# Optimization experiments

Hardware: AMD Instinct MI355X
Metric: run time of the kernel (lower is better)

## Reference

```python
import jax, jax.numpy as jnp
import numpy as np

NUM_GRAPHS = 32   # point clouds per batch
PTS = 1024        # points per cloud (equal-size graphs; batch = node_idx // PTS)
NUM_FEAT = 14
DIM = 64
K = 30            # kNN includes the self-edge (distance 0), as torch_cluster.knn does


def _edge_conv(xb, W1, b1, W2, b2):
    # xb: [B, P, F] node features, per-graph dynamic kNN EdgeConv with max aggregation
    s = jnp.sum(xb * xb, axis=-1)                                   # [B, P]
    d = s[:, :, None] + s[:, None, :] - 2.0 * jnp.einsum('bpf,bqf->bpq', xb, xb)
    idx = jax.lax.top_k(-d, K)[1]                                   # [B, P, K]
    xj = jax.vmap(lambda xg, ig: xg[ig])(xb, idx)                   # [B, P, K, F]
    xi = xb[:, :, None, :]
    e = jnp.concatenate([jnp.broadcast_to(xi, xj.shape), xj - xi], axis=-1)  # [B,P,K,2F]
    h = jax.nn.relu(e @ W1 + b1)
    h = jax.nn.relu(h @ W2 + b2)
    return jnp.max(h, axis=2)                                       # [B, P, DIM]


def setup_inputs() -> dict:
    key = jax.random.key(0)
    ks = jax.random.split(key, 24)
    N = NUM_GRAPHS * PTS

    def w(i, shape):
        scale = shape[0] ** -0.5 if len(shape) > 1 else 0.02
        return jax.random.normal(ks[i], shape, jnp.float32) * scale

    return dict(
        x=jax.random.normal(ks[0], (N, NUM_FEAT), jnp.float32),
        batch=jnp.arange(N, dtype=jnp.int32) // PTS,
        c1w1=w(1, (2 * NUM_FEAT, DIM)), c1b1=w(2, (DIM,)), c1w2=w(3, (DIM, DIM)), c1b2=w(4, (DIM,)),
        c2w1=w(5, (2 * DIM, DIM)), c2b1=w(6, (DIM,)), c2w2=w(7, (DIM, DIM)), c2b2=w(8, (DIM,)),
        c3w1=w(9, (2 * DIM, DIM)), c3b1=w(10, (DIM,)), c3w2=w(11, (DIM, DIM)), c3b2=w(12, (DIM,)),
        lw=w(13, (3 * DIM, 1024)), lb=w(14, (1024,)),
        hw1=w(15, (1024, 256)), hb1=w(16, (256,)),
        hw2=w(17, (256, 128)), hb2=w(18, (128,)),
        hw3=w(19, (128, DIM)), hb3=w(20, (DIM,)),
    )


def reference(x, batch, c1w1, c1b1, c1w2, c1b2, c2w1, c2b1, c2w2, c2b2,
              c3w1, c3b1, c3w2, c3b2, lw, lb, hw1, hb1, hw2, hb2, hw3, hb3):
    # batch encodes equal-size graphs of PTS nodes -> reshape to [B, P, F]
    xb = x.reshape(NUM_GRAPHS, PTS, -1)
    x1 = _edge_conv(xb, c1w1, c1b1, c1w2, c1b2)
    x2 = _edge_conv(x1, c2w1, c2b1, c2w2, c2b2)
    x3 = _edge_conv(x2, c3w1, c3b1, c3w2, c3b2)
    h = jnp.concatenate([x1, x2, x3], axis=-1).reshape(-1, 3 * DIM)  # [N, 192]
    h = jax.nn.relu(h @ lw + lb)      # lin1: MLP([3*dim, 1024])
    h = jax.nn.relu(h @ hw1 + hb1)    # MLP([1024, 256]); dropout = identity at eval
    h = jax.nn.relu(h @ hw2 + hb2)    # MLP([256, 128]); dropout = identity at eval
    return h @ hw3 + hb3              # Lin(128, dim)
```

## Files before the change

### kernel.cpp

```cpp
#include <hip/hip_runtime.h>
#include <hip/hip_bf16.h>
#include <float.h>

#define NG    32
#define PTS   1024
#define NPTS  (NG*PTS)
#define KNN   30
#define DIM   64
#define CHUNK 8192

typedef __attribute__((ext_vector_type(8))) short bf16x8;
typedef __attribute__((ext_vector_type(4))) float f32x4;
typedef unsigned short ushort_t;

__device__ inline void bfsplit(float v, ushort_t& h, ushort_t& l) {
    __hip_bfloat16 bh = __float2bfloat16(v);
    float r = v - __bfloat162float(bh);
    __hip_bfloat16 bl = __float2bfloat16(r);
    h = *reinterpret_cast<ushort_t*>(&bh);
    l = *reinterpret_cast<ushort_t*>(&bl);
}

template<int F>
__global__ __launch_bounds__(256) void prep_k(const float* __restrict__ X, int ldx,
                                              float* __restrict__ S32,
                                              double* __restrict__ S64,
                                              float* __restrict__ XT) {
    int p = blockIdx.x * 256 + threadIdx.x;
    float s32 = 0.f;
    double s64 = 0.0;
    #pragma unroll
    for (int f = 0; f < F; ++f) {
        float v = X[(size_t)p * ldx + f];
        s32 = fmaf(v, v, s32);
        s64 = fma((double)v, (double)v, s64);
        XT[(size_t)f * NPTS + p] = v;
    }
    S32[p] = s32;
    S64[p] = s64;
}

__global__ __launch_bounds__(256) void smax_k(const float* __restrict__ S32,
                                              float* __restrict__ SMAX,
                                              int* __restrict__ ovf_cnt) {
    if (blockIdx.x == 0 && threadIdx.x == 0) *ovf_cnt = 0;
    int g = blockIdx.x;
    int lane = threadIdx.x & 63, wv = threadIdx.x >> 6;
    float m = 0.f;
    for (int t = threadIdx.x; t < PTS; t += 256) m = fmaxf(m, S32[(size_t)g * PTS + t]);
    #pragma unroll
    for (int off = 32; off; off >>= 1) m = fmaxf(m, __shfl_xor(m, off));
    __shared__ float wm[4];
    if (lane == 0) wm[wv] = m;
    __syncthreads();
    if (threadIdx.x == 0)
        SMAX[g] = fmaxf(fmaxf(wm[0], wm[1]), fmaxf(wm[2], wm[3]));
}

template<int F>
__global__ __launch_bounds__(256) void knn_k(const float* __restrict__ X, int ldx,
                                             const float* __restrict__ XT,
                                             const float* __restrict__ S32,
                                             const double* __restrict__ S64,
                                             const float* __restrict__ SMAX,
                                             int* __restrict__ IDX,
                                             int* __restrict__ ovf_cnt,
                                             int* __restrict__ ovf_list) {
    constexpr int FP = (F + 3) & ~3;
    int wv = threadIdx.x >> 6;
    int lane = threadIdx.x & 63;
    int i0 = blockIdx.x * 16;
    int base = i0 & ~(PTS - 1);
    __shared__ __align__(16) float xis[16][FP];
    __shared__ int surv[4][4][64];
    for (int l = threadIdx.x; l < 16 * F; l += 256) {
        int pt = l / F, f = l - pt * F;
        xis[pt][f] = X[(size_t)(i0 + pt) * ldx + f];
    }
    __syncthreads();

    float si[4];
    #pragma unroll
    for (int ii = 0; ii < 4; ++ii) si[ii] = S32[i0 + wv * 4 + ii];
    float smax = SMAX[i0 >> 10];

    float d32[4][16];
    #pragma unroll
    for (int ii = 0; ii < 4; ++ii)
        #pragma unroll
        for (int r = 0; r < 16; ++r) d32[ii][r] = 0.f;

    constexpr int F4 = F & ~3;
    for (int f4 = 0; f4 < F4; f4 += 4) {
        float4 xi[4];
        #pragma unroll
        for (int ii = 0; ii < 4; ++ii)
            xi[ii] = *reinterpret_cast<const float4*>(&xis[wv * 4 + ii][f4]);
        #pragma unroll
        for (int fo = 0; fo < 4; ++fo) {
            int f = f4 + fo;
            #pragma unroll
            for (int m = 0; m < 4; ++m) {
                const float4 xj = *reinterpret_cast<const float4*>(
                    &XT[(size_t)f * NPTS + base + (m << 8) + (lane << 2)]);
                #pragma unroll
                for (int ii = 0; ii < 4; ++ii) {
                    float xif = (fo == 0) ? xi[ii].x : (fo == 1) ? xi[ii].y
                               : (fo == 2) ? xi[ii].z : xi[ii].w;
                    d32[ii][m * 4 + 0] = fmaf(xif, xj.x, d32[ii][m * 4 + 0]);
                    d32[ii][m * 4 + 1] = fmaf(xif, xj.y, d32[ii][m * 4 + 1]);
                    d32[ii][m * 4 + 2] = fmaf(xif, xj.z, d32[ii][m * 4 + 2]);
                    d32[ii][m * 4 + 3] = fmaf(xif, xj.w, d32[ii][m * 4 + 3]);
                }
            }
        }
    }
    for (int f = F4; f < F; ++f) {
        float xif[4];
        #pragma unroll
        for (int ii = 0; ii < 4; ++ii) xif[ii] = xis[wv * 4 + ii][f];
        #pragma unroll
        for (int m = 0; m < 4; ++m) {
            const float4 xj = *reinterpret_cast<const float4*>(
                &XT[(size_t)f * NPTS + base + (m << 8) + (lane << 2)]);
            #pragma unroll
            for (int ii = 0; ii < 4; ++ii) {
                d32[ii][m * 4 + 0] = fmaf(xif[ii], xj.x, d32[ii][m * 4 + 0]);
                d32[ii][m * 4 + 1] = fmaf(xif[ii], xj.y, d32[ii][m * 4 + 1]);
                d32[ii][m * 4 + 2] = fmaf(xif[ii], xj.z, d32[ii][m * 4 + 2]);
                d32[ii][m * 4 + 3] = fmaf(xif[ii], xj.w, d32[ii][m * 4 + 3]);
            }
        }
    }
    #pragma unroll
    for (int m = 0; m < 4; ++m) {
        const float4 sj = *reinterpret_cast<const float4*>(&S32[base + (m << 8) + (lane << 2)]);
        #pragma unroll
        for (int ii = 0; ii < 4; ++ii) {
            d32[ii][m * 4 + 0] = (si[ii] + sj.x) - 2.f * d32[ii][m * 4 + 0];
            d32[ii][m * 4 + 1] = (si[ii] + sj.y) - 2.f * d32[ii][m * 4 + 1];
            d32[ii][m * 4 + 2] = (si[ii] + sj.z) - 2.f * d32[ii][m * 4 + 2];
            d32[ii][m * 4 + 3] = (si[ii] + sj.w) - 2.f * d32[ii][m * 4 + 3];
        }
    }

    const unsigned long long below = (1ull << lane) - 1;
    #pragma unroll
    for (int ii = 0; ii < 4; ++ii) {
        int i = i0 + wv * 4 + ii;
        float lo = -1.f, hi = 2.f * (si[ii] + smax) + 1.f;
        for (int it = 0; it < 32; ++it) {
            float piv = 0.5f * (lo + hi);
            int cnt = 0;
            #pragma unroll
            for (int r = 0; r < 16; ++r)
                cnt += __popcll(__ballot(d32[ii][r] <= piv));
            if (cnt >= KNN) { hi = piv; if (cnt <= 56) break; }
            else lo = piv;
        }
        float T = hi + 1.6e-5f * (si[ii] + smax);

        int total = 0;
        #pragma unroll
        for (int r = 0; r < 16; ++r) {
            bool pred = d32[ii][r] <= T;
            unsigned long long mask = __ballot(pred);
            if (pred) {
                int slot = total + __popcll(mask & below);
                if (slot < 64)
                    surv[wv][ii][slot] = ((r >> 2) << 8) + (lane << 2) + (r & 3);
            }
            total += __popcll(mask);
        }
        if (total > 64) {
            if (lane == 0) ovf_list[atomicAdd(ovf_cnt, 1)] = i;
            continue;
        }
        __builtin_amdgcn_wave_barrier();
        asm volatile("s_waitcnt lgkmcnt(0)" ::: "memory");

        double d64 = DBL_MAX;
        int jabs = 0x7fffffff;
        if (lane < total) {
            int jl = surv[wv][ii][lane];
            jabs = base + jl;
            const float* xj = X + (size_t)jabs * ldx;
            double dot = 0.0;
            #pragma unroll
            for (int f = 0; f < F; ++f)
                dot = fma((double)xis[wv * 4 + ii][f], (double)xj[f], dot);
            d64 = (S64[i] + S64[jabs]) - 2.0 * dot;
        }
        #pragma unroll
        for (int k = 2; k <= 64; k <<= 1) {
            #pragma unroll
            for (int s = k >> 1; s > 0; s >>= 1) {
                double od = __shfl_xor(d64, s);
                int oj = __shfl_xor(jabs, s);
                bool otherSmaller = (od < d64) || (od == d64 && oj < jabs);
                bool keepSmaller = (((lane & k) == 0) == ((lane & s) == 0));
                if (otherSmaller == keepSmaller) { d64 = od; jabs = oj; }
            }
        }
        if (lane < KNN) IDX[(size_t)i * KNN + lane] = jabs;
        __builtin_amdgcn_wave_barrier();
    }
}

template<int F>
__global__ __launch_bounds__(256) void fb_k(const float* __restrict__ X, int ldx,
                                            const float* __restrict__ XT,
                                            const double* __restrict__ S64,
                                            int* __restrict__ IDX,
                                            const int* __restrict__ ovf_cnt,
                                            const int* __restrict__ ovf_list) {
    int wv = threadIdx.x >> 6, lane = threadIdx.x & 63;
    int novf = *ovf_cnt;
    __shared__ double xis[4][F];
    for (int t = blockIdx.x * 4 + wv; t < novf; t += 64 * 4) {
        int i = ovf_list[t];
        int base = i & ~(PTS - 1);
        if (lane < F) xis[wv][lane] = (double)X[(size_t)i * ldx + lane];
        __builtin_amdgcn_wave_barrier();
        asm volatile("s_waitcnt lgkmcnt(0)" ::: "memory");
        double dd[16];
        #pragma unroll
        for (int m = 0; m < 4; ++m) {
            int j0 = (m << 8) + (lane << 2);
            double d0 = 0.0, d1 = 0.0, d2 = 0.0, d3 = 0.0;
            #pragma unroll
            for (int f = 0; f < F; ++f) {
                double xif = xis[wv][f];
                const float4 xj = *reinterpret_cast<const float4*>(&XT[(size_t)f * NPTS + base + j0]);
                d0 = fma(xif, (double)xj.x, d0);
                d1 = fma(xif, (double)xj.y, d1);
                d2 = fma(xif, (double)xj.z, d2);
                d3 = fma(xif, (double)xj.w, d3);
            }
            dd[m * 4 + 0] = (S64[i] + S64[base + j0 + 0]) - 2.0 * d0;
            dd[m * 4 + 1] = (S64[i] + S64[base + j0 + 1]) - 2.0 * d1;
            dd[m * 4 + 2] = (S64[i] + S64[base + j0 + 2]) - 2.0 * d2;
            dd[m * 4 + 3] = (S64[i] + S64[base + j0 + 3]) - 2.0 * d3;
        }
        for (int k = 0; k < KNN; ++k) {
            double bd = DBL_MAX;
            int bj = 0x7fffffff;
            #pragma unroll
            for (int r = 0; r < 16; ++r) {
                int j = ((r >> 2) << 8) + (lane << 2) + (r & 3);
                if (dd[r] < bd) { bd = dd[r]; bj = j; }
            }
            #pragma unroll
            for (int off = 32; off; off >>= 1) {
                double od = __shfl_xor(bd, off);
                int oj = __shfl_xor(bj, off);
                if (od < bd || (od == bd && oj < bj)) { bd = od; bj = oj; }
            }
            if (((bj >> 2) & 63) == lane) {
                int r = ((bj >> 8) << 2) | (bj & 3);
                #pragma unroll
                for (int rr = 0; rr < 16; ++rr) if (rr == r) dd[rr] = DBL_MAX;
            }
            if (lane == 0) IDX[(size_t)i * KNN + k] = base + bj;
        }
        __builtin_amdgcn_wave_barrier();
    }
}

template<int F>
__global__ __launch_bounds__(256) void mg_k(const float* __restrict__ X, int ldx,
                                            const float* __restrict__ W1,
                                            const float* __restrict__ B1,
                                            float* __restrict__ Mo, float* __restrict__ Go) {
    int tid = blockIdx.x * 256 + threadIdx.x;
    int pp = tid >> 6, c = tid & 63;
    float m = B1[c], g = 0.f;
    #pragma unroll
    for (int f = 0; f < F; ++f) {
        float xv = X[(size_t)pp * ldx + f];
        float wt = W1[f * DIM + c];
        float wb = W1[(F + f) * DIM + c];
        m = fmaf(xv, wt - wb, m);
        g = fmaf(xv, wb, g);
    }
    Mo[(size_t)pp * DIM + c] = m;
    Go[(size_t)pp * DIM + c] = g;
}

__global__ __launch_bounds__(256) void edge_k(const int* __restrict__ IDX,
                                              const float* __restrict__ G,
                                              const float* __restrict__ Mb,
                                              const float* __restrict__ W2,
                                              const float* __restrict__ B2,
                                              float* __restrict__ OUT, int ldo) {
    __shared__ ushort_t w2hi[64][72], w2lo[64][72];
    __shared__ ushort_t h1hi[4][32][72], h1lo[4][32][72];
    int wv = threadIdx.x >> 6, lane = threadIdx.x & 63;
    int i = blockIdx.x * 4 + wv;
    int col16 = lane & 15, grp = lane >> 4, grp8 = (lane >> 4) << 3;

    for (int l = threadIdx.x; l < 4096; l += 256) {
        int c = l & 63, k = l >> 6;
        bfsplit(W2[k * 64 + c], w2hi[c][k], w2lo[c][k]);
    }
    __syncthreads();

    float mi = Mb[(size_t)i * DIM + lane];
    const int* idxrow = IDX + (size_t)i * KNN;
    int idxv = (lane < KNN) ? idxrow[lane] : 0;
    float g[KNN];
    #pragma unroll
    for (int nb = 0; nb < KNN; ++nb) {
        int j = __shfl(idxv, nb);
        g[nb] = G[(size_t)j * DIM + lane];
    }
    #pragma unroll
    for (int nb = 0; nb < KNN; ++nb) {
        float h = fmaxf(mi + g[nb], 0.f);
        bfsplit(h, h1hi[wv][nb][lane], h1lo[wv][nb][lane]);
    }
    h1hi[wv][30][lane] = 0; h1lo[wv][30][lane] = 0;
    h1hi[wv][31][lane] = 0; h1lo[wv][31][lane] = 0;
    __builtin_amdgcn_wave_barrier();
    asm volatile("s_waitcnt lgkmcnt(0)" ::: "memory");

    bf16x8 ahi[2][2], alo[2][2];
    #pragma unroll
    for (int m = 0; m < 2; ++m)
        #pragma unroll
        for (int ks = 0; ks < 2; ++ks) {
            ahi[m][ks] = *reinterpret_cast<const bf16x8*>(&h1hi[wv][m * 16 + col16][ks * 32 + grp8]);
            alo[m][ks] = *reinterpret_cast<const bf16x8*>(&h1lo[wv][m * 16 + col16][ks * 32 + grp8]);
        }

    float myout = 0.f;
    #pragma unroll
    for (int n = 0; n < 4; ++n) {
        bf16x8 bhi[2], blo[2];
        #pragma unroll
        for (int ks = 0; ks < 2; ++ks) {
            bhi[ks] = *reinterpret_cast<const bf16x8*>(&w2hi[n * 16 + col16][ks * 32 + grp8]);
            blo[ks] = *reinterpret_cast<const bf16x8*>(&w2lo[n * 16 + col16][ks * 32 + grp8]);
        }
        f32x4 acc0 = {0.f, 0.f, 0.f, 0.f}, acc1 = {0.f, 0.f, 0.f, 0.f};
        #pragma unroll
        for (int ks = 0; ks < 2; ++ks) {
            acc0 = __builtin_amdgcn_mfma_f32_16x16x32_bf16(ahi[0][ks], bhi[ks], acc0, 0, 0, 0);
            acc1 = __builtin_amdgcn_mfma_f32_16x16x32_bf16(ahi[1][ks], bhi[ks], acc1, 0, 0, 0);
            acc0 = __builtin_amdgcn_mfma_f32_16x16x32_bf16(ahi[0][ks], blo[ks], acc0, 0, 0, 0);
            acc1 = __builtin_amdgcn_mfma_f32_16x16x32_bf16(ahi[1][ks], blo[ks], acc1, 0, 0, 0);
            acc0 = __builtin_amdgcn_mfma_f32_16x16x32_bf16(alo[0][ks], bhi[ks], acc0, 0, 0, 0);
            acc1 = __builtin_amdgcn_mfma_f32_16x16x32_bf16(alo[1][ks], bhi[ks], acc1, 0, 0, 0);
        }
        float cm = fmaxf(fmaxf(acc0[0], acc0[1]), fmaxf(acc0[2], acc0[3]));
        cm = fmaxf(cm, fmaxf(acc1[0], acc1[1]));
        if (grp < 3) cm = fmaxf(cm, fmaxf(acc1[2], acc1[3]));
        cm = fmaxf(cm, __shfl_xor(cm, 16));
        cm = fmaxf(cm, __shfl_xor(cm, 32));
        if (grp == n) myout = cm;
    }
    OUT[(size_t)i * ldo + lane] = fmaxf(myout + B2[lane], 0.f);
}

__global__ __launch_bounds__(256) void wcvt_k(const float* __restrict__ W, int K, int N,
                                              ushort_t* __restrict__ Th,
                                              ushort_t* __restrict__ Tl) {
    int idx = blockIdx.x * 256 + threadIdx.x;
    if (idx >= K * N) return;
    int k = idx / N, n = idx - k * N;
    ushort_t h, l;
    bfsplit(W[idx], h, l);
    Th[(size_t)n * K + k] = h;
    Tl[(size_t)n * K + k] = l;
}

template<bool A32, bool OUT16, bool RELU>
__global__ __launch_bounds__(256) void gemmx_k(
    const float* __restrict__ Afp,
    const ushort_t* __restrict__ Agh, const ushort_t* __restrict__ Agl, int Kd,
    const ushort_t* __restrict__ Bth, const ushort_t* __restrict__ Btl,
    int N, const float* __restrict__ Bias,
    float* __restrict__ Cfp, ushort_t* __restrict__ Cgh, ushort_t* __restrict__ Cgl) {
    constexpr int BM = 128, BN = 128, BKP = 40;
    __shared__ ushort_t Ah[BM][BKP], Al[BM][BKP], Bh[BN][BKP], Bl[BN][BKP];
    int tid = threadIdx.x;
    int lane = tid & 63, wv = tid >> 6;
    int wr = wv >> 1, wc = wv & 1;
    int col16 = lane & 15, grp = lane >> 4, grp8 = grp << 3;
    int bm = blockIdx.y * BM, bn = blockIdx.x * BN;
    f32x4 acc[4][4];
    #pragma unroll
    for (int mf = 0; mf < 4; ++mf)
        #pragma unroll
        for (int nf = 0; nf < 4; ++nf) acc[mf][nf] = (f32x4){0.f, 0.f, 0.f, 0.f};

    for (int k0 = 0; k0 < Kd; k0 += 32) {
        if constexpr (A32) {
            for (int l = tid; l < BM * 8; l += 256) {
                int r = l >> 3, c4 = (l & 7) << 2;
                const float4 a = *reinterpret_cast<const float4*>(&Afp[(size_t)(bm + r) * Kd + k0 + c4]);
                ushort4 h4, l4;
                bfsplit(a.x, h4.x, l4.x);
                bfsplit(a.y, h4.y, l4.y);
                bfsplit(a.z, h4.z, l4.z);
                bfsplit(a.w, h4.w, l4.w);
                *reinterpret_cast<ushort4*>(&Ah[r][c4]) = h4;
                *reinterpret_cast<ushort4*>(&Al[r][c4]) = l4;
            }
        } else {
            for (int l = tid; l < BM * 4; l += 256) {
                int r = l >> 2, q = (l & 3) << 3;
                *reinterpret_cast<uint4*>(&Ah[r][q]) =
                    *reinterpret_cast<const uint4*>(&Agh[(size_t)(bm + r) * Kd + k0 + q]);
                *reinterpret_cast<uint4*>(&Al[r][q]) =
                    *reinterpret_cast<const uint4*>(&Agl[(size_t)(bm + r) * Kd + k0 + q]);
            }
        }
        for (int l = tid; l < BN * 4; l += 256) {
            int n = l >> 2, q = (l & 3) << 3;
            *reinterpret_cast<uint4*>(&Bh[n][q]) =
                *reinterpret_cast<const uint4*>(&Bth[(size_t)(bn + n) * Kd + k0 + q]);
            *reinterpret_cast<uint4*>(&Bl[n][q]) =
                *reinterpret_cast<const uint4*>(&Btl[(size_t)(bn + n) * Kd + k0 + q]);
        }
        __syncthreads();

        bf16x8 afh[4], afl[4], bfh[4], bfl[4];
        #pragma unroll
        for (int mf = 0; mf < 4; ++mf) {
            afh[mf] = *reinterpret_cast<const bf16x8*>(&Ah[wr * 64 + mf * 16 + col16][grp8]);
            afl[mf] = *reinterpret_cast<const bf16x8*>(&Al[wr * 64 + mf * 16 + col16][grp8]);
        }
        #pragma unroll
        for (int nf = 0; nf < 4; ++nf) {
            bfh[nf] = *reinterpret_cast<const bf16x8*>(&Bh[wc * 64 + nf * 16 + col16][grp8]);
            bfl[nf] = *reinterpret_cast<const bf16x8*>(&Bl[wc * 64 + nf * 16 + col16][grp8]);
        }
        #pragma unroll
        for (int mf = 0; mf < 4; ++mf)
            #pragma unroll
            for (int nf = 0; nf < 4; ++nf) {
                acc[mf][nf] = __builtin_amdgcn_mfma_f32_16x16x32_bf16(afh[mf], bfh[nf], acc[mf][nf], 0, 0, 0);
                acc[mf][nf] = __builtin_amdgcn_mfma_f32_16x16x32_bf16(afh[mf], bfl[nf], acc[mf][nf], 0, 0, 0);
                acc[mf][nf] = __builtin_amdgcn_mfma_f32_16x16x32_bf16(afl[mf], bfh[nf], acc[mf][nf], 0, 0, 0);
            }
        __syncthreads();
    }

    #pragma unroll
    for (int nf = 0; nf < 4; ++nf) {
        int col = bn + wc * 64 + nf * 16 + col16;
        float b = Bias[col];
        #pragma unroll
        for (int mf = 0; mf < 4; ++mf) {
            #pragma unroll
            for (int rg = 0; rg < 4; ++rg) {
                int row = bm + wr * 64 + mf * 16 + grp * 4 + rg;
                float v = acc[mf][nf][rg] + b;
                if (RELU) v = fmaxf(v, 0.f);
                if constexpr (OUT16) {
                    bfsplit(v, Cgh[(size_t)row * N + col], Cgl[(size_t)row * N + col]);
                } else {
                    Cfp[(size_t)row * N + col] = v;
                }
            }
        }
    }
}

template<int TM, int TN, int BK, bool RELU>
__global__ __launch_bounds__(256) void gemm_k(const float* __restrict__ A, int Kd,
                                              const float* __restrict__ W, int N,
                                              const float* __restrict__ Bias,
                                              float* __restrict__ C) {
    constexpr int MM = TM / 16, MN = TN / 16;
    __shared__ __align__(16) float As_t[BK][TM + 4];
    __shared__ __align__(16) float Ws[BK][TN];
    int bm = blockIdx.y * TM, bn = blockIdx.x * TN;
    int tid = threadIdx.x;
    int tr = tid >> 4, tc = tid & 15;
    float acc[MM][MN] = {};
    for (int k0 = 0; k0 < Kd; k0 += BK) {
        #pragma unroll
        for (int l = tid; l < TM * (BK / 4); l += 256) {
            int r = l / (BK / 4), q = l & (BK / 4 - 1);
            const float4 a4 = *reinterpret_cast<const float4*>(&A[(size_t)(bm + r) * Kd + k0 + 4 * q]);
            As_t[4 * q + 0][r] = a4.x;
            As_t[4 * q + 1][r] = a4.y;
            As_t[4 * q + 2][r] = a4.z;
            As_t[4 * q + 3][r] = a4.w;
        }
        #pragma unroll
        for (int l = tid; l < BK * (TN / 4); l += 256) {
            int r = l / (TN / 4), q = l & (TN / 4 - 1);
            *reinterpret_cast<float4*>(&Ws[r][4 * q]) =
                *reinterpret_cast<const float4*>(&W[(size_t)(k0 + r) * N + bn + 4 * q]);
        }
        __syncthreads();
        #pragma unroll
        for (int kk = 0; kk < BK; ++kk) {
            float a[MM], w[MN];
            #pragma unroll
            for (int u = 0; u < MM; u += 4) {
                const float4 v4 = *reinterpret_cast<const float4*>(&As_t[kk][tr * MM + u]);
                a[u] = v4.x; a[u + 1] = v4.y; a[u + 2] = v4.z; a[u + 3] = v4.w;
            }
            #pragma unroll
            for (int v = 0; v < MN; v += 4) {
                const float4 v4 = *reinterpret_cast<const float4*>(&Ws[kk][tc * MN + v]);
                w[v] = v4.x; w[v + 1] = v4.y; w[v + 2] = v4.z; w[v + 3] = v4.w;
            }
            #pragma unroll
            for (int u = 0; u < MM; ++u)
                #pragma unroll
                for (int v = 0; v < MN; ++v)
                    acc[u][v] = fmaf(a[u], w[v], acc[u][v]);
        }
        __syncthreads();
    }
    #pragma unroll
    for (int u = 0; u < MM; ++u) {
        int row = bm + tr * MM + u;
        #pragma unroll
        for (int v = 0; v < MN; v += 4) {
            int col = bn + tc * MN + v;
            float4 o;
            o.x = acc[u][v + 0] + Bias[col + 0];
            o.y = acc[u][v + 1] + Bias[col + 1];
            o.z = acc[u][v + 2] + Bias[col + 2];
            o.w = acc[u][v + 3] + Bias[col + 3];
            if (RELU) {
                o.x = fmaxf(o.x, 0.f); o.y = fmaxf(o.y, 0.f);
                o.z = fmaxf(o.z, 0.f); o.w = fmaxf(o.w, 0.f);
            }
            *reinterpret_cast<float4*>(&C[(size_t)row * N + col]) = o;
        }
    }
}

template<int F>
static void run_conv(const float* Xin, int ldx,
                     const float* W1, const float* B1,
                     const float* W2, const float* B2,
                     float* OUT, int ldo,
                     float* XT, float* S32, double* S64, float* SMAX,
                     float* Mb, float* Gb, int* IDX,
                     int* ovf_cnt, int* ovf_list,
                     hipStream_t stream) {
    prep_k<F><<<NPTS / 256, 256, 0, stream>>>(Xin, ldx, S32, S64, XT);
    smax_k<<<NG, 256, 0, stream>>>(S32, SMAX, ovf_cnt);
    knn_k<F><<<NPTS / 16, 256, 0, stream>>>(Xin, ldx, XT, S32, S64, SMAX, IDX,
                                            ovf_cnt, ovf_list);
    fb_k<F><<<64, 256, 0, stream>>>(Xin, ldx, XT, S64, IDX, ovf_cnt, ovf_list);
    mg_k<F><<<NPTS * DIM / 256, 256, 0, stream>>>(Xin, ldx, W1, B1, Mb, Gb);
    edge_k<<<NPTS / 4, 256, 0, stream>>>(IDX, Gb, Mb, W2, B2, OUT, ldo);
}

extern "C" void kernel_launch(void* const* d_in, const int* in_sizes, int n_in,
                              void* d_out, int out_size, void* d_ws, size_t ws_size,
                              hipStream_t stream) {
    (void)in_sizes; (void)n_in; (void)out_size; (void)ws_size;
    const float* x    = (const float*)d_in[0];
    const float* c1w1 = (const float*)d_in[2];  const float* c1b1 = (const float*)d_in[3];
    const float* c1w2 = (const float*)d_in[4];  const float* c1b2 = (const float*)d_in[5];
    const float* c2w1 = (const float*)d_in[6];  const float* c2b1 = (const float*)d_in[7];
    const float* c2w2 = (const float*)d_in[8];  const float* c2b2 = (const float*)d_in[9];
    const float* c3w1 = (const float*)d_in[10]; const float* c3b1 = (const float*)d_in[11];
    const float* c3w2 = (const float*)d_in[12]; const float* c3b2 = (const float*)d_in[13];
    const float* lw   = (const float*)d_in[14]; const float* lb   = (const float*)d_in[15];
    const float* hw1  = (const float*)d_in[16]; const float* hb1  = (const float*)d_in[17];
    const float* hw2  = (const float*)d_in[18]; const float* hb2  = (const float*)d_in[19];
    const float* hw3  = (const float*)d_in[20]; const float* hb3  = (const float*)d_in[21];
    float* out = (float*)d_out;

    float* XC  = (float*)d_ws;
    int*   IDX = (int*)(XC + (size_t)NPTS * 192);
    int*   ovf_cnt  = IDX + (size_t)NPTS * KNN;
    int*   ovf_list = ovf_cnt + 1;
    float* SCR = (float*)(ovf_list + NPTS + 1);
    float*  XT   = SCR;
    double* S64  = (double*)(XT + (size_t)64 * NPTS);
    float*  S32  = (float*)(S64 + NPTS);
    float*  SMAX = S32 + NPTS;
    float*  Mb   = SMAX + 64;
    float*  Gb   = Mb + (size_t)NPTS * DIM;
    ushort_t* H1h = (ushort_t*)SCR;
    ushort_t* H1l = H1h + (size_t)CHUNK * 1024;
    float* H2 = (float*)(H1l + (size_t)CHUNK * 1024);
    float* H3 = (float*)H1h;
    ushort_t* Wlwh = (ushort_t*)(H2 + (size_t)CHUNK * 256);
    ushort_t* Wlwl = Wlwh + 192 * 1024;
    ushort_t* Wh1h = Wlwl + 192 * 1024;
    ushort_t* Wh1l = Wh1h + 1024 * 256;

    run_conv<14>(x,        14,  c1w1, c1b1, c1w2, c1b2, XC + 0,   192,
                 XT, S32, S64, SMAX, Mb, Gb, IDX, ovf_cnt, ovf_list, stream);
    run_conv<64>(XC + 0,   192, c2w1, c2b1, c2w2, c2b2, XC + 64,  192,
                 XT, S32, S64, SMAX, Mb, Gb, IDX, ovf_cnt, ovf_list, stream);
    run_conv<64>(XC + 64,  192, c3w1, c3b1, c3w2, c3b2, XC + 128, 192,
                 XT, S32, S64, SMAX, Mb, Gb, IDX, ovf_cnt, ovf_list, stream);

    wcvt_k<<<(192 * 1024 + 255) / 256, 256, 0, stream>>>(lw,  192,  1024, Wlwh, Wlwl);
    wcvt_k<<<(1024 * 256 + 255) / 256, 256, 0, stream>>>(hw1, 1024, 256,  Wh1h, Wh1l);

    for (int ch = 0; ch < 4; ++ch) {
        const float* a0 = XC + (size_t)ch * CHUNK * 192;
        float* o0 = out + (size_t)ch * CHUNK * 64;
        gemmx_k<true, true, true><<<dim3(1024 / 128, CHUNK / 128), 256, 0, stream>>>(
            a0, nullptr, nullptr, 192, Wlwh, Wlwl, 1024, lb, nullptr, H1h, H1l);
        gemmx_k<false, false, true><<<dim3(256 / 128, CHUNK / 128), 256, 0, stream>>>(
            nullptr, H1h, H1l, 1024, Wh1h, Wh1l, 256, hb1, H2, nullptr, nullptr);
        gemm_k<64, 128, 16, true ><<<dim3(128 / 128, CHUNK / 64), 256, 0, stream>>>(H2, 256, hw2, 128, hb2, H3);
        gemm_k<64, 64, 16, false><<<dim3(64 / 64,   CHUNK / 64), 256, 0, stream>>>(H3, 128, hw3, 64,  hb3, o0);
    }
}
```

Measured before the change: 1.397 ms.

## Compute kNN distance matrices with split-bf16 MFMA in a separate kernel

Moves the pairwise distance computation out of the fused kNN kernel into a new dist_k kernel. It uses bf16 hi/lo split MFMA (three products) on a bf16-converted copy of the features and writes the full per-graph distance matrix to a global buffer in chunks of 4 graphs. The selection kernel then reads distances from that buffer instead of computing them with scalar FMAs. To absorb the lower precision, the candidate threshold margin is widened. The change adds global memory traffic (a 16MB D buffer per chunk written then read) and more kernel launches, and the reduced precision may push more rows into the fallback path.

```diff
diff --git a/kernel.cpp b/kernel.cpp
--- a/kernel.cpp
+++ b/kernel.cpp
@@ -8,6 +8,7 @@
 #define KNN   30
 #define DIM   64
 #define CHUNK 8192
+#define NGC   4
 
 typedef __attribute__((ext_vector_type(8))) short bf16x8;
 typedef __attribute__((ext_vector_type(4))) float f32x4;
@@ -21,11 +22,13 @@
     l = *reinterpret_cast<ushort_t*>(&bl);
 }
 
-template<int F>
+template<int F, int KP>
 __global__ __launch_bounds__(256) void prep_k(const float* __restrict__ X, int ldx,
                                               float* __restrict__ S32,
                                               double* __restrict__ S64,
-                                              float* __restrict__ XT) {
+                                              float* __restrict__ XT,
+                                              ushort_t* __restrict__ Xh,
+                                              ushort_t* __restrict__ Xl) {
     int p = blockIdx.x * 256 + threadIdx.x;
     float s32 = 0.f;
     double s64 = 0.0;
@@ -35,6 +38,12 @@
         s32 = fmaf(v, v, s32);
         s64 = fma((double)v, (double)v, s64);
         XT[(size_t)f * NPTS + p] = v;
+        bfsplit(v, Xh[(size_t)p * KP + f], Xl[(size_t)p * KP + f]);
+    }
+    #pragma unroll
+    for (int f = F; f < KP; ++f) {
+        Xh[(size_t)p * KP + f] = 0;
+        Xl[(size_t)p * KP + f] = 0;
     }
     S32[p] = s32;
     S64[p] = s64;
@@ -57,90 +66,94 @@
         SMAX[g] = fmaxf(fmaxf(wm[0], wm[1]), fmaxf(wm[2], wm[3]));
 }
 
+template<int KP>
+__global__ __launch_bounds__(256) void dist_k(const ushort_t* __restrict__ Xh,
+                                              const ushort_t* __restrict__ Xl,
+                                              const float* __restrict__ S32,
+                                              float* __restrict__ D,
+                                              int gbase) {
+    constexpr int KS = KP / 32;
+    int lane = threadIdx.x & 63, wv = threadIdx.x >> 6;
+    int wr = wv >> 1, wc = wv & 1;
+    int col16 = lane & 15, grp = lane >> 4, grp8 = grp << 3;
+    int gz = blockIdx.z;
+    int p0 = (gbase + gz) * PTS;
+    int bm = blockIdx.y * 128, bn = blockIdx.x * 128;
+
+    bf16x8 ah[4][KS], al[4][KS];
+    float4 si4[4];
+    #pragma unroll
+    for (int mf = 0; mf < 4; ++mf) {
+        int r = bm + wr * 64 + mf * 16 + col16;
+        #pragma unroll
+        for (int ks = 0; ks < KS; ++ks) {
+            ah[mf][ks] = *reinterpret_cast<const bf16x8*>(&Xh[(size_t)(p0 + r) * KP + ks * 32 + grp8]);
+            al[mf][ks] = *reinterpret_cast<const bf16x8*>(&Xl[(size_t)(p0 + r) * KP + ks * 32 + grp8]);
+        }
+        si4[mf] = *reinterpret_cast<const float4*>(&S32[p0 + bm + wr * 64 + mf * 16 + grp * 4]);
+    }
+    #pragma unroll
+    for (int nf = 0; nf < 4; ++nf) {
+        int c = bn + wc * 64 + nf * 16 + col16;
+        bf16x8 bh[KS], bl[KS];
+        #pragma unroll
+        for (int ks = 0; ks < KS; ++ks) {
+            bh[ks] = *reinterpret_cast<const bf16x8*>(&Xh[(size_t)(p0 + c) * KP + ks * 32 + grp8]);
+            bl[ks] = *reinterpret_cast<const bf16x8*>(&Xl[(size_t)(p0 + c) * KP + ks * 32 + grp8]);
+        }
+        float sj = S32[p0 + c];
+        #pragma unroll
+        for (int mf = 0; mf < 4; ++mf) {
+            f32x4 acc = {0.f, 0.f, 0.f, 0.f};
+            #pragma unroll
+            for (int ks = 0; ks < KS; ++ks) {
+                acc = __builtin_amdgcn_mfma_f32_16x16x32_bf16(ah[mf][ks], bh[ks], acc, 0, 0, 0);
+                acc = __builtin_amdgcn_mfma_f32_16x16x32_bf16(ah[mf][ks], bl[ks], acc, 0, 0, 0);
+                acc = __builtin_amdgcn_mfma_f32_16x16x32_bf16(al[mf][ks], bh[ks], acc, 0, 0, 0);
+            }
+            size_t rowbase = (size_t)(gz * PTS + bm + wr * 64 + mf * 16 + grp * 4);
+            #pragma unroll
+            for (int rg = 0; rg < 4; ++rg)
+                D[(rowbase + rg) * 1024 + bn + wc * 64 + nf * 16 + col16] =
+                    (si4[mf][rg] + sj) - 2.f * acc[rg];
+        }
+    }
+}
+
 template<int F>
-__global__ __launch_bounds__(256) void knn_k(const float* __restrict__ X, int ldx,
-                                             const float* __restrict__ XT,
+__global__ __launch_bounds__(256) void sel_k(const float* __restrict__ X, int ldx,
+                                             const float* __restrict__ D,
                                              const float* __restrict__ S32,
                                              const double* __restrict__ S64,
                                              const float* __restrict__ SMAX,
                                              int* __restrict__ IDX,
                                              int* __restrict__ ovf_cnt,
-                                             int* __restrict__ ovf_list) {
-    constexpr int FP = (F + 3) & ~3;
-    int wv = threadIdx.x >> 6;
-    int lane = threadIdx.x & 63;
-    int i0 = blockIdx.x * 16;
+                                             int* __restrict__ ovf_list,
+                                             int gbase) {
+    int wv = threadIdx.x >> 6, lane = threadIdx.x & 63;
+    int l0 = blockIdx.x * 16;
+    int i0 = gbase * PTS + l0;
     int base = i0 & ~(PTS - 1);
-    __shared__ __align__(16) float xis[16][FP];
+    __shared__ float xis[16][F];
     __shared__ int surv[4][4][64];
     for (int l = threadIdx.x; l < 16 * F; l += 256) {
         int pt = l / F, f = l - pt * F;
         xis[pt][f] = X[(size_t)(i0 + pt) * ldx + f];
     }
     __syncthreads();
+    float smax = SMAX[i0 >> 10];
 
     float si[4];
-    #pragma unroll
-    for (int ii = 0; ii < 4; ++ii) si[ii] = S32[i0 + wv * 4 + ii];
-    float smax = SMAX[i0 >> 10];
-
     float d32[4][16];
     #pragma unroll
-    for (int ii = 0; ii < 4; ++ii)
-        #pragma unroll
-        for (int r = 0; r < 16; ++r) d32[ii][r] = 0.f;
-
-    constexpr int F4 = F & ~3;
-    for (int f4 = 0; f4 < F4; f4 += 4) {
-        float4 xi[4];
-        #pragma unroll
-        for (int ii = 0; ii < 4; ++ii)
-            xi[ii] = *reinterpret_cast<const float4*>(&xis[wv * 4 + ii][f4]);
-        #pragma unroll
-        for (int fo = 0; fo < 4; ++fo) {
-            int f = f4 + fo;
-            #pragma unroll
-            for (int m = 0; m < 4; ++m) {
-                const float4 xj = *reinterpret_cast<const float4*>(
-                    &XT[(size_t)f * NPTS + base + (m << 8) + (lane << 2)]);
-                #pragma unroll
-                for (int ii = 0; ii < 4; ++ii) {
-                    float xif = (fo == 0) ? xi[ii].x : (fo == 1) ? xi[ii].y
-                               : (fo == 2) ? xi[ii].z : xi[ii].w;
-                    d32[ii][m * 4 + 0] = fmaf(xif, xj.x, d32[ii][m * 4 + 0]);
-                    d32[ii][m * 4 + 1] = fmaf(xif, xj.y, d32[ii][m * 4 + 1]);
-                    d32[ii][m * 4 + 2] = fmaf(xif, xj.z, d32[ii][m * 4 + 2]);
-                    d32[ii][m * 4 + 3] = fmaf(xif, xj.w, d32[ii][m * 4 + 3]);
-                }
-            }
-        }
-    }
-    for (int f = F4; f < F; ++f) {
-        float xif[4];
-        #pragma unroll
-        for (int ii = 0; ii < 4; ++ii) xif[ii] = xis[wv * 4 + ii][f];
+    for (int ii = 0; ii < 4; ++ii) {
+        si[ii] = S32[i0 + wv * 4 + ii];
         #pragma unroll
         for (int m = 0; m < 4; ++m) {
-            const float4 xj = *reinterpret_cast<const float4*>(
-                &XT[(size_t)f * NPTS + base + (m << 8) + (lane << 2)]);
-            #pragma unroll
-            for (int ii = 0; ii < 4; ++ii) {
-                d32[ii][m * 4 + 0] = fmaf(xif[ii], xj.x, d32[ii][m * 4 + 0]);
-                d32[ii][m * 4 + 1] = fmaf(xif[ii], xj.y, d32[ii][m * 4 + 1]);
-                d32[ii][m * 4 + 2] = fmaf(xif[ii], xj.z, d32[ii][m * 4 + 2]);
-                d32[ii][m * 4 + 3] = fmaf(xif[ii], xj.w, d32[ii][m * 4 + 3]);
-            }
-        }
-    }
-    #pragma unroll
-    for (int m = 0; m < 4; ++m) {
-        const float4 sj = *reinterpret_cast<const float4*>(&S32[base + (m << 8) + (lane << 2)]);
-        #pragma unroll
-        for (int ii = 0; ii < 4; ++ii) {
-            d32[ii][m * 4 + 0] = (si[ii] + sj.x) - 2.f * d32[ii][m * 4 + 0];
-            d32[ii][m * 4 + 1] = (si[ii] + sj.y) - 2.f * d32[ii][m * 4 + 1];
-            d32[ii][m * 4 + 2] = (si[ii] + sj.z) - 2.f * d32[ii][m * 4 + 2];
-            d32[ii][m * 4 + 3] = (si[ii] + sj.w) - 2.f * d32[ii][m * 4 + 3];
+            const float4 v = *reinterpret_cast<const float4*>(
+                &D[(size_t)(l0 + wv * 4 + ii) * 1024 + (m << 8) + (lane << 2)]);
+            d32[ii][m * 4 + 0] = v.x; d32[ii][m * 4 + 1] = v.y;
+            d32[ii][m * 4 + 2] = v.z; d32[ii][m * 4 + 3] = v.w;
         }
     }
 
@@ -158,7 +171,7 @@
             if (cnt >= KNN) { hi = piv; if (cnt <= 56) break; }
             else lo = piv;
         }
-        float T = hi + 1.6e-5f * (si[ii] + smax);
+        float T = hi + 1.0e-4f * (si[ii] + smax);
 
         int total = 0;
         #pragma unroll
@@ -538,19 +551,23 @@
     }
 }
 
-template<int F>
+template<int F, int KP>
 static void run_conv(const float* Xin, int ldx,
                      const float* W1, const float* B1,
                      const float* W2, const float* B2,
                      float* OUT, int ldo,
                      float* XT, float* S32, double* S64, float* SMAX,
+                     ushort_t* Xbh, ushort_t* Xbl, float* Dbuf,
                      float* Mb, float* Gb, int* IDX,
                      int* ovf_cnt, int* ovf_list,
                      hipStream_t stream) {
-    prep_k<F><<<NPTS / 256, 256, 0, stream>>>(Xin, ldx, S32, S64, XT);
+    prep_k<F, KP><<<NPTS / 256, 256, 0, stream>>>(Xin, ldx, S32, S64, XT, Xbh, Xbl);
     smax_k<<<NG, 256, 0, stream>>>(S32, SMAX, ovf_cnt);
-    knn_k<F><<<NPTS / 16, 256, 0, stream>>>(Xin, ldx, XT, S32, S64, SMAX, IDX,
-                                            ovf_cnt, ovf_list);
+    for (int c = 0; c < NG / NGC; ++c) {
+        dist_k<KP><<<dim3(8, 8, NGC), 256, 0, stream>>>(Xbh, Xbl, S32, Dbuf, c * NGC);
+        sel_k<F><<<NGC * PTS / 16, 256, 0, stream>>>(Xin, ldx, Dbuf, S32, S64, SMAX,
+                                                     IDX, ovf_cnt, ovf_list, c * NGC);
+    }
     fb_k<F><<<64, 256, 0, stream>>>(Xin, ldx, XT, S64, IDX, ovf_cnt, ovf_list);
     mg_k<F><<<NPTS * DIM / 256, 256, 0, stream>>>(Xin, ldx, W1, B1, Mb, Gb);
     edge_k<<<NPTS / 4, 256, 0, stream>>>(IDX, Gb, Mb, W2, B2, OUT, ldo);
@@ -577,13 +594,16 @@
     int*   IDX = (int*)(XC + (size_t)NPTS * 192);
     int*   ovf_cnt  = IDX + (size_t)NPTS * KNN;
     int*   ovf_list = ovf_cnt + 1;
-    float* SCR = (float*)(ovf_list + NPTS + 1);
-    float*  XT   = SCR;
-    double* S64  = (double*)(XT + (size_t)64 * NPTS);
-    float*  S32  = (float*)(S64 + NPTS);
-    float*  SMAX = S32 + NPTS;
-    float*  Mb   = SMAX + 64;
-    float*  Gb   = Mb + (size_t)NPTS * DIM;
+    float* SCR = (float*)(ovf_list + NPTS + 3);
+    float*    XT   = SCR;
+    double*   S64  = (double*)(XT + (size_t)64 * NPTS);
+    float*    S32  = (float*)(S64 + NPTS);
+    float*    SMAX = S32 + NPTS;
+    ushort_t* Xbh  = (ushort_t*)(SMAX + 64);
+    ushort_t* Xbl  = Xbh + (size_t)NPTS * 64;
+    float*    Dbuf = (float*)(Xbl + (size_t)NPTS * 64);
+    float*    Mb   = Dbuf;
+    float*    Gb   = Mb + (size_t)NPTS * DIM;
     ushort_t* H1h = (ushort_t*)SCR;
     ushort_t* H1l = H1h + (size_t)CHUNK * 1024;
     float* H2 = (float*)(H1l + (size_t)CHUNK * 1024);
@@ -593,12 +613,12 @@
     ushort_t* Wh1h = Wlwl + 192 * 1024;
     ushort_t* Wh1l = Wh1h + 1024 * 256;
 
-    run_conv<14>(x,        14,  c1w1, c1b1, c1w2, c1b2, XC + 0,   192,
-                 XT, S32, S64, SMAX, Mb, Gb, IDX, ovf_cnt, ovf_list, stream);
-    run_conv<64>(XC + 0,   192, c2w1, c2b1, c2w2, c2b2, XC + 64,  192,
-                 XT, S32, S64, SMAX, Mb, Gb, IDX, ovf_cnt, ovf_list, stream);
-    run_conv<64>(XC + 64,  192, c3w1, c3b1, c3w2, c3b2, XC + 128, 192,
-                 XT, S32, S64, SMAX, Mb, Gb, IDX, ovf_cnt, ovf_list, stream);
+    run_conv<14, 32>(x,        14,  c1w1, c1b1, c1w2, c1b2, XC + 0,   192,
+                     XT, S32, S64, SMAX, Xbh, Xbl, Dbuf, Mb, Gb, IDX, ovf_cnt, ovf_list, stream);
+    run_conv<64, 64>(XC + 0,   192, c2w1, c2b1, c2w2, c2b2, XC + 64,  192,
+                     XT, S32, S64, SMAX, Xbh, Xbl, Dbuf, Mb, Gb, IDX, ovf_cnt, ovf_list, stream);
+    run_conv<64, 64>(XC + 64,  192, c3w1, c3b1, c3w2, c3b2, XC + 128, 192,
+                     XT, S32, S64, SMAX, Xbh, Xbl, Dbuf, Mb, Gb, IDX, ovf_cnt, ovf_list, stream);
 
     wcvt_k<<<(192 * 1024 + 255) / 256, 256, 0, stream>>>(lw,  192,  1024, Wlwh, Wlwl);
     wcvt_k<<<(1024 * 256 + 255) / 256, 256, 0, stream>>>(hw1, 1024, 256,  Wh1h, Wh1l);
```

New measurement: 1.858 ms. +33.0%, slower.
